# Kernel tuning notes

Hardware: AMD Instinct MI355X
Metric: run time of the kernel (lower is better)

## Reference

```python
import jax, jax.numpy as jnp
import numpy as np
from jax import lax

OVERLAP_THRESHOLD = 0.5


def _pairwise_iou(a, b):
    # a: [A,4], b: [B,4] -> [A,B]  (jaccard() in the original repo)
    max_xy = jnp.minimum(a[:, None, 2:], b[None, :, 2:])
    min_xy = jnp.maximum(a[:, None, :2], b[None, :, :2])
    wh = jnp.clip(max_xy - min_xy, 0.0)
    inter = wh[..., 0] * wh[..., 1]
    area_a = (a[:, 2] - a[:, 0]) * (a[:, 3] - a[:, 1])
    area_b = (b[:, 2] - b[:, 0]) * (b[:, 3] - b[:, 1])
    union = area_a[:, None] + area_b[None, :] - inter
    return inter / union


def _elementwise_iou(a, b):
    # matches UBR_ZERO_IoULoss._intersect/_iou_loss: same-shape [K,4] boxes
    max_xy = jnp.minimum(a[:, 2:], b[:, 2:])
    min_xy = jnp.maximum(a[:, :2], b[:, :2])
    wh = jnp.clip(max_xy - min_xy, 0.0)
    inter = wh[:, 0] * wh[:, 1]
    area_a = (a[:, 2] - a[:, 0]) * (a[:, 3] - a[:, 1])
    area_b = (b[:, 2] - b[:, 0]) * (b[:, 3] - b[:, 1])
    return inter / (area_a + area_b - inter)


def _inverse_transform(boxes, deltas):
    w = boxes[:, 2] - boxes[:, 0] + 1.0
    h = boxes[:, 3] - boxes[:, 1] + 1.0
    cx = boxes[:, 0] + 0.5 * w
    cy = boxes[:, 1] + 0.5 * h
    pcx = deltas[:, 0] * w + cx
    pcy = deltas[:, 1] * h + cy
    pw = jnp.exp(deltas[:, 2]) * w
    ph = jnp.exp(deltas[:, 3]) * h
    return jnp.stack([pcx - 0.5 * pw, pcy - 0.5 * ph,
                      pcx + 0.5 * pw, pcy + 0.5 * ph], axis=1)


def setup_inputs() -> dict:
    key = jax.random.key(0)
    k1, k2, k3, k4 = jax.random.split(key, 4)
    N, M, D = 32768, 4096, 512
    raw = jax.random.uniform(k1, (N, 4), dtype=jnp.float32)
    xy = raw[:, :2] * 900.0
    wh = raw[:, 2:] * 100.0 + 1.0
    rois = jnp.concatenate([xy, xy + wh], axis=1)
    # gt boxes = jittered subset of rois -> guarantees IoU>0.5 matches exist
    gt_box = rois[:M] + jax.random.normal(k2, (M, 4), dtype=jnp.float32) * 2.0
    bbox_pred = jax.random.normal(k3, (N, 4), dtype=jnp.float32) * 0.1
    feat = jax.random.normal(k4, (N, D), dtype=jnp.float32)
    return {"rois": rois, "bbox_pred": bbox_pred, "gt_box": gt_box, "feat": feat}


def reference(rois, bbox_pred, gt_box, feat):
    num_rois = rois.shape[0]
    iou = _pairwise_iou(rois, gt_box)              # [N, M]
    max_iou = jnp.max(iou, axis=1)                 # [N]
    max_gt_idx = jnp.argmax(iou, axis=1)           # [N]
    # boolean compaction in torch replaced by a fixed-shape mask (jit-safe)
    mask = lax.stop_gradient((max_iou > OVERLAP_THRESHOLD).astype(rois.dtype))
    n_matched = jnp.sum(mask).astype(jnp.int32)
    matched_gt = gt_box[max_gt_idx]                # [N, 4]
    refined = _inverse_transform(rois, bbox_pred)  # [N, 4]
    iou_ref = _elementwise_iou(refined, matched_gt)
    loss = -jnp.log(iou_ref + 0.1) * mask          # per-roi, 0 where unmatched
    feat_loss = jnp.sum(jnp.abs(jnp.sum(feat * mask[:, None], axis=0)))
    return loss, n_matched, num_rois, refined * mask[:, None], feat_loss
```

## Files before the change

kernel.cpp:

```cpp
#include <hip/hip_runtime.h>
#include <math.h>

#define GRID 16
#define NCELL 256
#define FB 128

typedef unsigned long long ull;

__device__ __forceinline__ int cell_xy(float c, int& out) {
  int v = (int)floorf((c + 16.0f) * 0.015625f);
  out = min(max(v, 0), GRID - 1);
  return out;
}

__global__ __launch_bounds__(256) void k_bin(
    const float4* __restrict__ gt4, int M,
    int* __restrict__ off_g, int* __restrict__ cnt_g,
    float4* __restrict__ gbox, float* __restrict__ garea,
    int* __restrict__ ctr) {
  __shared__ int scnt[NCELL], spre[NCELL], sfill[NCELL];
  const int t = threadIdx.x;
  scnt[t] = 0;
  __syncthreads();
  for (int k = t; k < M; k += 256) {
    float4 g = gt4[k];
    int ix, iy;
    cell_xy(0.5f * (g.x + g.z), ix);
    cell_xy(0.5f * (g.y + g.w), iy);
    atomicAdd(&scnt[iy * GRID + ix], 1);
  }
  __syncthreads();
  int v = scnt[t];
  spre[t] = v; __syncthreads();
  for (int o = 1; o < NCELL; o <<= 1) {
    int a = (t >= o) ? spre[t - o] : 0; __syncthreads();
    spre[t] += a; __syncthreads();
  }
  int ex = spre[t] - v;
  off_g[t] = ex; cnt_g[t] = v; sfill[t] = ex;
  __syncthreads();
  for (int k = t; k < M; k += 256) {
    float4 g = gt4[k];
    int ix, iy;
    cell_xy(0.5f * (g.x + g.z), ix);
    cell_xy(0.5f * (g.y + g.w), iy);
    int pos = atomicAdd(&sfill[iy * GRID + ix], 1);
    gbox[pos] = g;
    garea[pos] = (g.z - g.x) * (g.w - g.y);
  }
  if (t == 0) *ctr = 0;
}

__global__ __launch_bounds__(128) void k_main(
    const float4* __restrict__ rois4, const float4* __restrict__ deltas4,
    const int* __restrict__ off_g, const int* __restrict__ cnt_g,
    const float4* __restrict__ gbox, const float* __restrict__ garea,
    int* __restrict__ ctr, int* __restrict__ mlist,
    float* __restrict__ out_loss, float* __restrict__ out_refined) {
  __shared__ int soff[NCELL], scnt_[NCELL];
  const int t = threadIdx.x;
  soff[t] = off_g[t];           scnt_[t] = cnt_g[t];
  soff[t + 128] = off_g[t + 128]; scnt_[t + 128] = cnt_g[t + 128];
  __syncthreads();

  const int i = blockIdx.x * 128 + t;
  float4 r = rois4[i];
  const float area_a = (r.z - r.x) * (r.w - r.y);
  int cx, cy;
  cell_xy(0.5f * (r.x + r.z), cx);
  cell_xy(0.5f * (r.y + r.w), cy);

  const double Cd = 0.500000029802322387695312500;
  float bi = 0.f, bu = 1.f;
  int bjpos = 0;
  bool matched = false;
  for (int dy = -1; dy <= 1; ++dy) {
    int yy = cy + dy;
    if (yy < 0 || yy > GRID - 1) continue;
    int c0 = (yy << 4) | max(cx - 1, 0);
    int c1 = (yy << 4) | min(cx + 1, GRID - 1);
    int s = soff[c0];
    int e = soff[c1] + scnt_[c1];
    for (int j = s; j < e; ++j) {
      float4 g = gbox[j];
      float ab = garea[j];
      float ix = fminf(r.z, g.z) - fmaxf(r.x, g.x);
      float iy = fminf(r.w, g.w) - fmaxf(r.y, g.y);
      float inter = fmaxf(ix, 0.f) * fmaxf(iy, 0.f);
      float uni = (area_a + ab) - inter;
      bool upos = uni > 0.f;
      float ug = upos ? uni : 3.0e38f;
      matched = matched | (fma(-Cd, (double)ug, (double)inter) > 0.0);
      bool win = upos && (inter * bu > bi * uni);
      bi = win ? inter : bi;
      bu = win ? uni : bu;
      bjpos = win ? j : bjpos;
    }
  }
  float m = matched ? 1.f : 0.f;
  if (matched) mlist[atomicAdd(ctr, 1)] = i;

  float4 d = deltas4[i];
  float w = r.z - r.x + 1.f, h = r.w - r.y + 1.f;
  float ccx = r.x + 0.5f * w, ccy = r.y + 0.5f * h;
  float pcx = d.x * w + ccx, pcy = d.y * h + ccy;
  float pw = expf(d.z) * w, ph = expf(d.w) * h;
  float rx0 = pcx - 0.5f * pw, ry0 = pcy - 0.5f * ph;
  float rx1 = pcx + 0.5f * pw, ry1 = pcy + 0.5f * ph;

  float loss = 0.f;
  if (matched) {
    float4 g = gbox[bjpos];
    float ix = fmaxf(fminf(rx1, g.z) - fmaxf(rx0, g.x), 0.f);
    float iy = fmaxf(fminf(ry1, g.w) - fmaxf(ry0, g.y), 0.f);
    float inter = ix * iy;
    float aa = (rx1 - rx0) * (ry1 - ry0);
    float ab = (g.z - g.x) * (g.w - g.y);
    float er = inter / (aa + ab - inter);
    loss = -logf(er + 0.1f);
  }
  out_loss[i] = loss;
  out_refined[4 * i + 0] = rx0 * m;
  out_refined[4 * i + 1] = ry0 * m;
  out_refined[4 * i + 2] = rx1 * m;
  out_refined[4 * i + 3] = ry1 * m;
}

__global__ __launch_bounds__(256) void k_feat2(
    const float4* __restrict__ feat4, const int* __restrict__ mlist,
    const int* __restrict__ ctr, float4* __restrict__ pcolsP4, int D4) {
  const int nm = *ctr;
  const int t = threadIdx.x;
  const int c = t & 127;
  const int h = t >> 7;
  __shared__ int sidx[256];

  const int chunk = (nm + FB - 1) / FB;
  const int start = blockIdx.x * chunk;
  int len = nm - start;
  len = (len < 0) ? 0 : ((len > chunk) ? chunk : len);
  for (int k = t; k < len; k += 256) sidx[k] = mlist[start + k];
  __syncthreads();

  float4 acc = {0.f, 0.f, 0.f, 0.f};
  int e0 = h * 8;
  for (; e0 + 8 <= len; e0 += 16) {
    int id[8];
    #pragma unroll
    for (int k = 0; k < 8; ++k) id[k] = sidx[e0 + k];
    float4 v[8];
    #pragma unroll
    for (int k = 0; k < 8; ++k) v[k] = feat4[(size_t)id[k] * D4 + c];
    #pragma unroll
    for (int k = 0; k < 8; ++k) {
      acc.x += v[k].x; acc.y += v[k].y; acc.z += v[k].z; acc.w += v[k].w;
    }
  }
  for (int e = e0; e < len && e < e0 + 8; ++e) {
    float4 v = feat4[(size_t)sidx[e] * D4 + c];
    acc.x += v.x; acc.y += v.y; acc.z += v.z; acc.w += v.w;
  }

  __shared__ float4 red[256];
  red[t] = acc;
  __syncthreads();
  if (t < 128) {
    float4 o = red[t + 128];
    acc.x += o.x; acc.y += o.y; acc.z += o.z; acc.w += o.w;
    pcolsP4[(size_t)blockIdx.x * 128 + t] = acc;
  }
}

__global__ __launch_bounds__(512) void k_final(
    const float* __restrict__ pcolsP, const int* __restrict__ ctr,
    float* __restrict__ out, int N) {
  const int t = threadIdx.x;
  float s = 0.f;
  for (int r = 0; r < FB; ++r) s += pcolsP[(size_t)r * 512 + t];
  float a = fabsf(s);
  for (int off = 32; off > 0; off >>= 1) a += __shfl_down(a, off, 64);
  __shared__ float ra[8];
  if ((t & 63) == 0) ra[t >> 6] = a;
  __syncthreads();
  if (t == 0) {
    float ta = 0.f;
    for (int k = 0; k < 8; ++k) ta += ra[k];
    out[N] = (float)(*ctr);
    out[N + 1] = (float)N;
    out[(size_t)5 * N + 2] = ta;
  }
}

extern "C" void kernel_launch(void* const* d_in, const int* in_sizes, int n_in,
                              void* d_out, int out_size, void* d_ws, size_t ws_size,
                              hipStream_t stream) {
  const float* rois = (const float*)d_in[0];
  const float* bbox = (const float*)d_in[1];
  const float* gt   = (const float*)d_in[2];
  const float* feat = (const float*)d_in[3];
  const int N = in_sizes[0] / 4;
  const int M = in_sizes[2] / 4;
  const int D = in_sizes[3] / N;
  float* out = (float*)d_out;

  char* ws = (char*)d_ws;
  int* off_g   = (int*)ws;
  int* cnt_g   = off_g + NCELL;
  int* ctr     = cnt_g + NCELL;
  int* mlist   = ctr + 13;
  float4* gbox = (float4*)(mlist + N);
  float* garea = (float*)(gbox + M);
  float* pcolsP = garea + M;

  k_bin<<<1, 256, 0, stream>>>((const float4*)gt, M, off_g, cnt_g,
                               gbox, garea, ctr);
  k_main<<<N / 128, 128, 0, stream>>>((const float4*)rois, (const float4*)bbox,
                                      off_g, cnt_g, gbox, garea, ctr, mlist,
                                      out, out + N + 2);
  k_feat2<<<FB, 256, 0, stream>>>((const float4*)feat, mlist, ctr,
                                  (float4*)pcolsP, D / 4);
  k_final<<<1, 512, 0, stream>>>(pcolsP, ctr, out, N);
}
```

Baseline: 179.8 us.

## Split per-ROI candidate scan across four lanes and double feature-reduction blocks

Each ROI is now handled by four lanes of a 256-thread block, each scanning a strided quarter of the neighbouring gt-cell candidates. The lanes then merge best-IoU and match state with xor shuffles, and lane 0 writes the outputs. This targets the long serial per-thread loop and low thread count of the main kernel. Separately, the feature-sum kernel uses 256 blocks instead of 128, with a smaller index buffer, to spread the gather over more work. The cost is shuffle overhead, idle lanes in the epilogue, and possible tie-break differences from the original first-index argmax order.

```diff
diff --git a/kernel.cpp b/kernel.cpp
--- a/kernel.cpp
+++ b/kernel.cpp
@@ -3,14 +3,13 @@
 
 #define GRID 16
 #define NCELL 256
-#define FB 128
+#define FB 256
 
 typedef unsigned long long ull;
 
-__device__ __forceinline__ int cell_xy(float c, int& out) {
+__device__ __forceinline__ void cell_xy(float c, int& out) {
   int v = (int)floorf((c + 16.0f) * 0.015625f);
   out = min(max(v, 0), GRID - 1);
-  return out;
 }
 
 __global__ __launch_bounds__(256) void k_bin(
@@ -51,7 +50,7 @@
   if (t == 0) *ctr = 0;
 }
 
-__global__ __launch_bounds__(128) void k_main(
+__global__ __launch_bounds__(256) void k_main(
     const float4* __restrict__ rois4, const float4* __restrict__ deltas4,
     const int* __restrict__ off_g, const int* __restrict__ cnt_g,
     const float4* __restrict__ gbox, const float* __restrict__ garea,
@@ -60,10 +59,11 @@
   __shared__ int soff[NCELL], scnt_[NCELL];
   const int t = threadIdx.x;
   soff[t] = off_g[t];           scnt_[t] = cnt_g[t];
-  soff[t + 128] = off_g[t + 128]; scnt_[t + 128] = cnt_g[t + 128];
-  __syncthreads();
-
-  const int i = blockIdx.x * 128 + t;
+  if (t < NCELL - 256) {}
+  __syncthreads();
+
+  const int slice = t & 3;
+  const int i = blockIdx.x * 64 + (t >> 2);
   float4 r = rois4[i];
   const float area_a = (r.z - r.x) * (r.w - r.y);
   int cx, cy;
@@ -81,7 +81,8 @@
     int c1 = (yy << 4) | min(cx + 1, GRID - 1);
     int s = soff[c0];
     int e = soff[c1] + scnt_[c1];
-    for (int j = s; j < e; ++j) {
+    #pragma unroll 2
+    for (int j = s + slice; j < e; j += 4) {
       float4 g = gbox[j];
       float ab = garea[j];
       float ix = fminf(r.z, g.z) - fmaxf(r.x, g.x);
@@ -97,8 +98,22 @@
       bjpos = win ? j : bjpos;
     }
   }
-  float m = matched ? 1.f : 0.f;
-  if (matched) mlist[atomicAdd(ctr, 1)] = i;
+  int mi = matched ? 1 : 0;
+  #pragma unroll
+  for (int x = 1; x <= 2; x <<= 1) {
+    float bi_o = __shfl_xor(bi, x, 64);
+    float bu_o = __shfl_xor(bu, x, 64);
+    int bj_o = __shfl_xor(bjpos, x, 64);
+    mi |= __shfl_xor(mi, x, 64);
+    bool take = bi_o * bu > bi * bu_o;
+    bi = take ? bi_o : bi;
+    bu = take ? bu_o : bu;
+    bjpos = take ? bj_o : bjpos;
+  }
+  if (slice != 0) return;
+  bool mt = mi != 0;
+  float m = mt ? 1.f : 0.f;
+  if (mt) mlist[atomicAdd(ctr, 1)] = i;
 
   float4 d = deltas4[i];
   float w = r.z - r.x + 1.f, h = r.w - r.y + 1.f;
@@ -109,7 +124,7 @@
   float rx1 = pcx + 0.5f * pw, ry1 = pcy + 0.5f * ph;
 
   float loss = 0.f;
-  if (matched) {
+  if (mt) {
     float4 g = gbox[bjpos];
     float ix = fmaxf(fminf(rx1, g.z) - fmaxf(rx0, g.x), 0.f);
     float iy = fmaxf(fminf(ry1, g.w) - fmaxf(ry0, g.y), 0.f);
@@ -133,7 +148,7 @@
   const int t = threadIdx.x;
   const int c = t & 127;
   const int h = t >> 7;
-  __shared__ int sidx[256];
+  __shared__ int sidx[128];
 
   const int chunk = (nm + FB - 1) / FB;
   const int start = blockIdx.x * chunk;
@@ -214,9 +229,9 @@
 
   k_bin<<<1, 256, 0, stream>>>((const float4*)gt, M, off_g, cnt_g,
                                gbox, garea, ctr);
-  k_main<<<N / 128, 128, 0, stream>>>((const float4*)rois, (const float4*)bbox,
-                                      off_g, cnt_g, gbox, garea, ctr, mlist,
-                                      out, out + N + 2);
+  k_main<<<N / 64, 256, 0, stream>>>((const float4*)rois, (const float4*)bbox,
+                                     off_g, cnt_g, gbox, garea, ctr, mlist,
+                                     out, out + N + 2);
   k_feat2<<<FB, 256, 0, stream>>>((const float4*)feat, mlist, ctr,
                                   (float4*)pcolsP, D / 4);
   k_final<<<1, 512, 0, stream>>>(pcolsP, ctr, out, N);
```

After: 164.5 us. -8.5%, faster.
